# Optimization experiments

Measured on AMD Instinct MI355X. Metric: run time of the kernel, lower is better.

## Reference

```python
import jax, jax.numpy as jnp
import numpy as np

B, N, DIM, H = 2, 1024, 512, 8
DK = DIM // H
HIDDEN = 16
EPS = 1e-6
BETA_NOT = 0.5


def setup_inputs() -> dict:
    key = jax.random.key(0)
    ks = jax.random.split(key, 8)
    s = 0.02
    return {
        "x": jax.random.normal(ks[0], (B, N, DIM), jnp.float32),
        "Wqkv0": jax.random.normal(ks[1], (DIM, 3 * DIM), jnp.float32) * s,
        "Wqkv1": jax.random.normal(ks[2], (DIM, 3 * DIM), jnp.float32) * s,
        "Wproj": jax.random.normal(ks[3], (DIM, DIM), jnp.float32) * s,
        "conv1_w": jax.random.normal(ks[4], (HIDDEN, 6), jnp.float32) * s,  # 1x1 conv, 6 in-ch
        "conv1_b": jnp.zeros((HIDDEN,), jnp.float32),
        "conv2_w": jax.random.normal(ks[5], (4, HIDDEN), jnp.float32) * s,  # 1x1 conv -> 4 gates
        "conv2_b": jnp.full((4,), -5.0, jnp.float32),  # gate_init='neutral': all biases -5
        "chain_value_logit": jnp.asarray(-2.0, jnp.float32),
    }


def reference(x, Wqkv0, Wqkv1, Wproj, conv1_w, conv1_b, conv2_w, conv2_b, chain_value_logit):
    scale = 1.0 / np.sqrt(DK).astype(np.float32)

    def qkv(W):
        t = (x @ W).reshape(B, N, 3, H, DK).transpose(2, 0, 3, 1, 4)  # [3,B,H,N,dk]
        return t[0], t[1], t[2]

    q0, k0, v0 = qkv(Wqkv0)
    q1, k1, v1 = qkv(Wqkv1)

    S0 = jnp.einsum('bhnd,bhmd->bhnm', q0, k0) * scale
    S1 = jnp.einsum('bhnd,bhmd->bhnm', q1, k1) * scale
    A0 = jax.nn.softmax(S0, axis=-1)
    A1 = jax.nn.softmax(S1, axis=-1)
    C_fwd = A0 @ A1
    C_bwd = A1 @ A0

    BtH = B * H
    S0i = S0.reshape(BtH, N, N)
    S1i = S1.reshape(BtH, N, N)
    Cri = jnp.log(C_fwd + EPS).reshape(BtH, N, N)
    Cli = jnp.log(C_bwd + EPS).reshape(BtH, N, N)
    # channels: [S1..SM, S1^T..SM^T, log C_fwd, log C_bwd]
    feat = jnp.stack([S0i, S1i, S0i.transpose(0, 2, 1), S1i.transpose(0, 2, 1), Cri, Cli], axis=1)

    # dense edge-gate head: 1x1 conv -> GELU(tanh) -> 1x1 conv -> sigmoid
    h1 = jax.nn.gelu(jnp.einsum('bcnm,oc->bonm', feat, conv1_w) + conv1_b[None, :, None, None],
                     approximate=True)
    gates = jax.nn.sigmoid(jnp.einsum('bcnm,oc->bonm', h1, conv2_w) + conv2_b[None, :, None, None])
    g_and, g_or, g_not, g_chain = gates[:, 0], gates[:, 1], gates[:, 2], gates[:, 3]

    lse_all = jnp.logaddexp(S0i, S1i)  # logsumexp over the 2 views
    # n_views=2: S_sum-S0 = S1, S_mean_others = S1
    Smix = S0i + g_and * S1i + g_or * (lse_all - S0i) - g_not * (BETA_NOT * S1i) + g_chain * Cri

    A = jax.nn.softmax(Smix.reshape(B, H, N, N), axis=-1)
    y_base = A @ v0
    y_chain = A0 @ (A1 @ v1)  # value-aware chain transport
    y = y_base + jax.nn.sigmoid(chain_value_logit) * y_chain
    y = y.transpose(0, 2, 1, 3).reshape(B, N, DIM)
    return y @ Wproj
```

## Files before the change

### kernel.cpp

```cpp
#include <hip/hip_runtime.h>
#include <math.h>
#include <stdio.h>


typedef unsigned short u16;
typedef __attribute__((ext_vector_type(8))) short short8;
typedef __attribute__((ext_vector_type(4))) short short4v;
typedef __attribute__((ext_vector_type(4))) float f32x4;
typedef __attribute__((ext_vector_type(2))) float f32x2;
typedef __attribute__((ext_vector_type(16))) float f32x16;

#define DEVI static __device__ __forceinline__

DEVI float bf2f(u16 u){ union{unsigned v; float f;} x; x.v = ((unsigned)u)<<16u; return x.f; }
DEVI u16 f2bf(float f){ union{float f; unsigned v;} x; x.f=f; unsigned r = x.v + 0x7FFFu + ((x.v>>16)&1u); return (u16)(r>>16); }

DEVI f32x2 bc(float s){ f32x2 r; r[0]=s; r[1]=s; return r; }
DEVI f32x2 pkfma(f32x2 a, f32x2 b, f32x2 c){ return __builtin_elementwise_fma(a,b,c); }
DEVI f32x2 pkmin(f32x2 a, f32x2 b){ return __builtin_elementwise_min(a,b); }
DEVI f32x2 pkmax(f32x2 a, f32x2 b){ return __builtin_elementwise_max(a,b); }

DEVI void gload_lds16(const u16* gptr, u16* lptr){
  __builtin_amdgcn_global_load_lds(
      (const __attribute__((address_space(1))) void*)gptr,
      (__attribute__((address_space(3))) void*)lptr,
      16, 0, 0);
}

enum { EPI_F32=0, EPI_BF16=1, EPI_LOGBF16=2, EPI_BF16T=3, EPI_QKV=4, EPI_Y=5 };

template<int BM,int BN,int WR,int WC,int EPI,int MODE>
__global__ __launch_bounds__(256) void gemm_bt(
    const u16* __restrict__ A, const u16* __restrict__ B,
    const u16* __restrict__ A2, const u16* __restrict__ B2,
    void* __restrict__ p0, void* __restrict__ p1, void* __restrict__ p2,
    void* __restrict__ p0b, void* __restrict__ p1b, void* __restrict__ p2b,
    const float* __restrict__ logit,
    int K, int lda, int ldb,
    long long sA, long long sB, long long sC, int ldc, int zsplit)
{
  constexpr int WM = BM/WR, WN = BN/WC;
  constexpr int MB = WM/32, NB = WN/32;
  constexpr int BK = 64;
  __shared__ u16 As[BM][BK];
  __shared__ u16 Bs[BN][BK];
  const int z = blockIdx.z;
  const bool sec = (MODE==1) && (z >= zsplit);
  const int ze = sec ? z - zsplit : z;
  const u16* Ap = (sec ? A2 : A) + (long long)ze*sA;
  const u16* Bp = (sec ? B2 : B) + (long long)ze*sB;
  void* o0 = sec ? p0b : p0;
  void* o1 = sec ? p1b : p1;
  void* o2 = sec ? p2b : p2;
  const int r0 = blockIdx.y*BM, c0 = blockIdx.x*BN;
  const int tid = threadIdx.x;
  const int wave = tid>>6, lane = tid&63;
  const int wr = (wave/WC)*WM, wc = (wave%WC)*WN;
  const int lrow = lane&31;
  const int kby  = (lane>>5)*16;
  const int l8 = lane>>3, l7 = lane&7;
  const int scol = ((l7 ^ l8) * 8);

  f32x16 acc[MB][NB] = {};

  auto kloop = [&](const u16* AP, const u16* BP){
    for (int k0=0; k0<K; k0+=BK){
      __syncthreads();
      #pragma unroll
      for (int i=0;i<BM/32;i++){
        int ins = wave + 4*i;
        int row = ins*8 + l8;
        gload_lds16(&AP[(long long)(r0+row)*lda + k0 + scol], &As[ins*8][0]);
      }
      #pragma unroll
      for (int i=0;i<BN/32;i++){
        int ins = wave + 4*i;
        int row = ins*8 + l8;
        gload_lds16(&BP[(long long)(c0+row)*ldb + k0 + scol], &Bs[ins*8][0]);
      }
      __syncthreads();
      #pragma unroll
      for (int kk=0; kk<4; ++kk){
        short8 af[MB], bfr[NB];
        #pragma unroll
        for (int m=0;m<MB;m++){
          int R = wr + m*32 + lrow;
          int eo = ((kk*32 + kby) ^ ((R&7)<<4)) >> 1;
          af[m] = *(const short8*)&As[R][eo];
        }
        #pragma unroll
        for (int n=0;n<NB;n++){
          int R = wc + n*32 + lrow;
          int eo = ((kk*32 + kby) ^ ((R&7)<<4)) >> 1;
          bfr[n] = *(const short8*)&Bs[R][eo];
        }
        #pragma unroll
        for (int m=0;m<MB;m++)
          #pragma unroll
          for (int n=0;n<NB;n++)
            acc[m][n] = __builtin_amdgcn_mfma_f32_32x32x16_bf16(af[m], bfr[n], acc[m][n], 0,0,0);
      }
    }
  };

  kloop(Ap, Bp);
  if constexpr (MODE==2){
    kloop(A2 + (long long)z*sA, B2 + (long long)z*sB);
  }

  float tscale = 1.f;
  if constexpr (EPI==EPI_BF16T){ if (logit) tscale = 1.f/(1.f+expf(-logit[0])); }

  #pragma unroll
  for (int m=0;m<MB;m++)
   #pragma unroll
   for (int n=0;n<NB;n++)
    #pragma unroll
    for (int reg=0;reg<16;reg++){
      int r = r0 + wr + m*32 + (reg&3) + 8*(reg>>2) + 4*(lane>>5);
      int c = c0 + wc + n*32 + lrow;
      float v = acc[m][n][reg];
      if constexpr (EPI==EPI_F32){
        ((float*)o0)[(long long)z*sC + (long long)r*ldc + c] = v;
      } else if constexpr (EPI==EPI_BF16){
        ((u16*)o0)[(long long)ze*sC + (long long)r*ldc + c] = f2bf(v);
      } else if constexpr (EPI==EPI_LOGBF16){
        ((u16*)o0)[(long long)z*sC + (long long)r*ldc + c] = f2bf(__logf(v + 1e-6f));
      } else if constexpr (EPI==EPI_BF16T){
        ((u16*)o0)[(long long)z*sC + (long long)c*ldc + r] = f2bf(v*tscale);
      } else if constexpr (EPI==EPI_QKV){
        int b = r>>10, n_ = r&1023;
        int which = c>>9, h = (c>>6)&7, d = c&63;
        long long bh = (long long)b*8 + h;
        if (which==0)      ((u16*)o0)[(bh*1024 + n_)*64 + d] = f2bf(v*0.125f);
        else if (which==1) ((u16*)o1)[(bh*1024 + n_)*64 + d] = f2bf(v);
        else               ((u16*)o2)[(bh*64 + d)*1024 + n_] = f2bf(v);
      } else if constexpr (EPI==EPI_Y){
        int b = z>>3, h = z&7;
        ((u16*)o0)[((long long)(b*1024 + r))*512 + h*64 + c] = f2bf(v);
      }
    }
}

__global__ __launch_bounds__(256) void softmaxT(
    const u16* __restrict__ Sa, u16* __restrict__ Aa, u16* __restrict__ ATa,
    const u16* __restrict__ Sb, u16* __restrict__ Ab2, u16* __restrict__ ATb)
{
  __shared__ u16 tile[32][1032];
  const int zz = blockIdx.y;
  const long long nn = 1048576;
  const u16* S; u16 *A; u16 *AT;
  if (zz < 16){ S = Sa + (long long)zz*nn;      A = Aa  + (long long)zz*nn;      AT = ATa + (long long)zz*nn; }
  else        { S = Sb + (long long)(zz-16)*nn; A = Ab2 + (long long)(zz-16)*nn; AT = ATb + (long long)(zz-16)*nn; }
  const int rb = blockIdx.x*32;
  const int tid = threadIdx.x;

  #pragma unroll
  for (int i=0;i<16;i++){
    int f = tid + i*256;
    int r = f>>7, c = (f&127)*8;
    *(short8*)&tile[r][c] = *(const short8*)&S[(long long)(rb+r)*1024 + c];
  }
  __syncthreads();

  const int row = ((tid>>6)<<3) + ((tid&63)>>3);
  const int seg = tid&7;
  float m = -3.4e38f;
  #pragma unroll
  for (int j=0;j<16;j++){
    short8 x = *(const short8*)&tile[row][seg*128 + j*8];
    #pragma unroll
    for (int q=0;q<8;q++) m = fmaxf(m, bf2f((u16)x[q]));
  }
  m = fmaxf(m, __shfl_xor(m,1,64));
  m = fmaxf(m, __shfl_xor(m,2,64));
  m = fmaxf(m, __shfl_xor(m,4,64));
  float s = 0.f;
  #pragma unroll
  for (int j=0;j<16;j++){
    short8 x = *(const short8*)&tile[row][seg*128 + j*8];
    #pragma unroll
    for (int q=0;q<8;q++) s += __expf(bf2f((u16)x[q]) - m);
  }
  s += __shfl_xor(s,1,64);
  s += __shfl_xor(s,2,64);
  s += __shfl_xor(s,4,64);
  float inv = 1.f/s;
  #pragma unroll
  for (int j=0;j<16;j++){
    short8 x = *(const short8*)&tile[row][seg*128 + j*8];
    short8 o;
    #pragma unroll
    for (int q=0;q<8;q++) o[q] = (short)f2bf(__expf(bf2f((u16)x[q]) - m)*inv);
    *(short8*)&tile[row][seg*128 + j*8] = o;
  }
  __syncthreads();
  #pragma unroll
  for (int i=0;i<16;i++){
    int f = tid + i*256;
    int r = f>>7, c = (f&127)*8;
    *(short8*)&A[(long long)(rb+r)*1024 + c] = *(const short8*)&tile[r][c];
  }
  #pragma unroll
  for (int i=0;i<4;i++){
    int c = tid*4 + i;
    short8 o0, o1, o2, o3;
    #pragma unroll
    for (int q=0;q<8;q++){
      o0[q] = (short)tile[q][c];
      o1[q] = (short)tile[8+q][c];
      o2[q] = (short)tile[16+q][c];
      o3[q] = (short)tile[24+q][c];
    }
    u16* dst = &AT[(long long)c*1024 + rb];
    *(short8*)&dst[0]  = o0;
    *(short8*)&dst[8]  = o1;
    *(short8*)&dst[16] = o2;
    *(short8*)&dst[24] = o3;
  }
}

__global__ __launch_bounds__(256) void softmax_rows2(
    const u16* __restrict__ s0, u16* __restrict__ d0,
    const u16* __restrict__ s1, u16* __restrict__ d1, int half)
{
  const int b = blockIdx.x;
  const u16* s; u16* a;
  if (b < half){ s = s0 + (long long)b*1024;        a = d0 + (long long)b*1024; }
  else         { s = s1 + (long long)(b-half)*1024; a = d1 + (long long)(b-half)*1024; }
  const int tid = threadIdx.x;
  short4v x = *(const short4v*)&s[tid*4];
  float v[4];
  #pragma unroll
  for (int i=0;i<4;i++) v[i] = bf2f((u16)x[i]);
  __shared__ float red[4];
  float m = fmaxf(fmaxf(v[0],v[1]),fmaxf(v[2],v[3]));
  #pragma unroll
  for (int off=32; off>0; off>>=1) m = fmaxf(m, __shfl_xor(m, off, 64));
  if ((tid&63)==0) red[tid>>6] = m;
  __syncthreads();
  m = fmaxf(fmaxf(red[0],red[1]),fmaxf(red[2],red[3]));
  float e[4], sum=0.f;
  #pragma unroll
  for (int i=0;i<4;i++){ e[i] = __expf(v[i]-m); sum += e[i]; }
  #pragma unroll
  for (int off=32; off>0; off>>=1) sum += __shfl_xor(sum, off, 64);
  __syncthreads();
  if ((tid&63)==0) red[tid>>6] = sum;
  __syncthreads();
  float inv = 1.f/(red[0]+red[1]+red[2]+red[3]);
  short4v o;
  #pragma unroll
  for (int i=0;i<4;i++) o[i] = (short)f2bf(e[i]*inv);
  *(short4v*)&a[tid*4] = o;
}

__global__ __launch_bounds__(256) void cast_f32_bf16(const float* __restrict__ in, u16* __restrict__ out, int n4)
{
  int i = blockIdx.x*256 + threadIdx.x;
  if (i < n4){
    f32x4 x = ((const f32x4*)in)[i];
    short4v o;
    #pragma unroll
    for (int j=0;j<4;j++) o[j] = (short)f2bf(x[j]);
    ((short4v*)out)[i] = o;
  }
}

__global__ __launch_bounds__(256) void castT_f32_bf16_2(
    const float* __restrict__ in0, u16* __restrict__ out0,
    const float* __restrict__ in1, u16* __restrict__ out1, int rows, int cols)
{
  __shared__ float tile[32][33];
  const float* in = blockIdx.z ? in1 : in0;
  u16* out        = blockIdx.z ? out1 : out0;
  const int cb = blockIdx.x*32, rb = blockIdx.y*32;
  const int tx = threadIdx.x&31, ty = threadIdx.x>>5;
  #pragma unroll
  for (int rr=0;rr<4;rr++){
    int i = ty + rr*8;
    tile[i][tx] = in[(long long)(rb+i)*cols + cb+tx];
  }
  __syncthreads();
  #pragma unroll
  for (int rr=0;rr<4;rr++){
    int i = ty + rr*8;
    out[(long long)(cb+i)*rows + rb+tx] = f2bf(tile[tx][i]);
  }
}

__global__ __launch_bounds__(256) void castT_f32_bf16(const float* __restrict__ in, u16* __restrict__ out, int rows, int cols)
{
  __shared__ float tile[32][33];
  const int cb = blockIdx.x*32, rb = blockIdx.y*32;
  const int tx = threadIdx.x&31, ty = threadIdx.x>>5;
  #pragma unroll
  for (int rr=0;rr<4;rr++){
    int i = ty + rr*8;
    tile[i][tx] = in[(long long)(rb+i)*cols + cb+tx];
  }
  __syncthreads();
  #pragma unroll
  for (int rr=0;rr<4;rr++){
    int i = ty + rr*8;
    out[(long long)(cb+i)*rows + rb+tx] = f2bf(tile[tx][i]);
  }
}

__global__ __launch_bounds__(256) void gating_kernel(
    const u16* __restrict__ S0, const u16* __restrict__ S1,
    const u16* __restrict__ CR, const u16* __restrict__ CL,
    const float* __restrict__ w1, const float* __restrict__ b1,
    const float* __restrict__ w2, const float* __restrict__ b2,
    u16* __restrict__ Smix)
{
  __shared__ float t0[32][33], t1[32][33], t0t[32][33], t1t[32][33];
  const int tid = threadIdx.x;
  const long long base = (long long)blockIdx.z*1024*1024;
  const int rb = blockIdx.y*32, cb = blockIdx.x*32;
  const int tx = tid&31, ty = tid>>5;
  #pragma unroll
  for (int rr=0;rr<4;rr++){
    int i = ty + rr*8;
    t0 [i][tx] = bf2f(S0[base + (long long)(rb+i)*1024 + cb+tx]);
    t1 [i][tx] = bf2f(S1[base + (long long)(rb+i)*1024 + cb+tx]);
    t0t[i][tx] = bf2f(S0[base + (long long)(cb+i)*1024 + rb+tx]);
    t1t[i][tx] = bf2f(S1[base + (long long)(cb+i)*1024 + rb+tx]);
  }
  __syncthreads();
  #pragma unroll 1
  for (int rr=0;rr<2;rr++){
    const int i0 = ty + rr*16, i1 = i0 + 8;
    f32x2 s0, s1v, s0t, s1t, cr, cl;
    s0[0]  = t0 [i0][tx]; s0[1]  = t0 [i1][tx];
    s1v[0] = t1 [i0][tx]; s1v[1] = t1 [i1][tx];
    s0t[0] = t0t[tx][i0]; s0t[1] = t0t[tx][i1];
    s1t[0] = t1t[tx][i0]; s1t[1] = t1t[tx][i1];
    long long off0 = base + (long long)(rb+i0)*1024 + cb+tx;
    long long off1 = base + (long long)(rb+i1)*1024 + cb+tx;
    cr[0] = bf2f(CR[off0]); cr[1] = bf2f(CR[off1]);
    cl[0] = bf2f(CL[off0]); cl[1] = bf2f(CL[off1]);
    f32x2 a0 = bc(b2[0]), a1 = bc(b2[1]), a2 = bc(b2[2]), a3 = bc(b2[3]);
    #pragma unroll 4
    for (int o=0;o<16;o++){
      f32x2 xx = pkfma(bc(w1[o*6+0]), s0,  bc(b1[o]));
      xx = pkfma(bc(w1[o*6+1]), s1v, xx);
      xx = pkfma(bc(w1[o*6+2]), s0t, xx);
      xx = pkfma(bc(w1[o*6+3]), s1t, xx);
      xx = pkfma(bc(w1[o*6+4]), cr,  xx);
      xx = pkfma(bc(w1[o*6+5]), cl,  xx);
      f32x2 xx2 = xx*xx;
      f32x2 u   = pkfma(bc(0.044715f), xx2, bc(1.f));
      f32x2 zz  = (xx*u) * bc(1.5957691f);
      zz = pkmin(pkmax(zz, bc(-3.f)), bc(3.f));
      f32x2 w   = pkfma(bc(-0.011008f), zz*zz, bc(0.25f));
      f32x2 p   = pkfma(zz, w, bc(0.5f));
      f32x2 hh  = xx*p;
      a0 = pkfma(bc(w2[o]),    hh, a0);
      a1 = pkfma(bc(w2[16+o]), hh, a1);
      a2 = pkfma(bc(w2[32+o]), hh, a2);
      a3 = pkfma(bc(w2[48+o]), hh, a3);
    }
    f32x2 g0, g1, g2, g3;
    { float E;
      E=__expf(a0[0]); g0[0]=E*(1.f-E);  E=__expf(a0[1]); g0[1]=E*(1.f-E);
      E=__expf(a1[0]); g1[0]=E*(1.f-E);  E=__expf(a1[1]); g1[1]=E*(1.f-E);
      E=__expf(a2[0]); g2[0]=E*(1.f-E);  E=__expf(a2[1]); g2[1]=E*(1.f-E);
      E=__expf(a3[0]); g3[0]=E*(1.f-E);  E=__expf(a3[1]); g3[1]=E*(1.f-E);
    }
    f32x2 mx = pkmax(s0, s1v);
    f32x2 dd = s0 - s1v;
    f32x2 ad = pkmax(dd, bc(0.f)-dd);
    f32x2 ee, lg;
    ee[0] = __expf(-ad[0]); ee[1] = __expf(-ad[1]);
    lg[0] = __logf(1.f+ee[0]); lg[1] = __logf(1.f+ee[1]);
    f32x2 lse = mx + lg;
    f32x2 smix = s0 + g0*s1v + g1*(lse - s0) - g2*(bc(0.5f)*s1v) + g3*cr;
    Smix[off0] = f2bf(smix[0]);
    Smix[off1] = f2bf(smix[1]);
  }
}

extern "C" void kernel_launch(void* const* d_in, const int* in_sizes, int n_in,
                              void* d_out, int out_size, void* d_ws, size_t ws_size,
                              hipStream_t stream)
{
  const float* x     = (const float*)d_in[0];
  const float* Wqkv0 = (const float*)d_in[1];
  const float* Wqkv1 = (const float*)d_in[2];
  const float* Wproj = (const float*)d_in[3];
  const float* c1w   = (const float*)d_in[4];
  const float* c1b   = (const float*)d_in[5];
  const float* c2w   = (const float*)d_in[6];
  const float* c2b   = (const float*)d_in[7];
  const float* logit = (const float*)d_in[8];

  char* ws = (char*)d_ws;
  size_t off = 0;
  auto alloc = [&](size_t bytes)->char*{ char* p = ws + off; off = (off + bytes + 255) & ~(size_t)255; return p; };

  const long long NN16 = 16LL*1024*1024;
  u16* xb  = (u16*)alloc(2048LL*512*2);
  u16* w0T = (u16*)alloc(1536LL*512*2);
  u16* w1T = (u16*)alloc(1536LL*512*2);
  u16* wpT = (u16*)alloc(512LL*512*2);
  u16* q0  = (u16*)alloc(16LL*1024*64*2);
  u16* k0  = (u16*)alloc(16LL*1024*64*2);
  u16* v0T = (u16*)alloc(16LL*1024*64*2);
  u16* q1  = (u16*)alloc(16LL*1024*64*2);
  u16* k1  = (u16*)alloc(16LL*1024*64*2);
  u16* v1T = (u16*)alloc(16LL*1024*64*2);
  u16* S0b = (u16*)alloc(NN16*2);
  u16* S1b = (u16*)alloc(NN16*2);
  u16* A0  = (u16*)alloc(NN16*2);
  u16* A1  = (u16*)alloc(NN16*2);
  u16* A0T = (u16*)alloc(NN16*2);
  u16* A1T = (u16*)alloc(NN16*2);
  u16* CL  = (u16*)alloc(NN16*2);
  u16* tT  = (u16*)alloc(16LL*64*1024*2);
  u16* Yb  = (u16*)alloc(2048LL*512*2);

  u16* CR   = A0T;
  u16* Smix = A1T;
  u16* Ab   = S0b;

  if (off > ws_size){
    fprintf(stderr, "kernel_launch: ws too small: need %zu have %zu\n", off, ws_size);
    return;
  }

  dim3 blk(256);

  cast_f32_bf16<<<dim3(262144/256), blk, 0, stream>>>(x, xb, 262144);
  castT_f32_bf16_2<<<dim3(48,16,2), blk, 0, stream>>>(Wqkv0, w0T, Wqkv1, w1T, 512, 1536);
  castT_f32_bf16<<<dim3(16,16), blk, 0, stream>>>(Wproj, wpT, 512, 512);

  gemm_bt<128,128,2,2,EPI_QKV,1><<<dim3(12,16,2), blk, 0, stream>>>(
      xb, w0T, xb, w1T, q0, k0, v0T, q1, k1, v1T, nullptr,
      512, 512, 512, 0, 0, 0, 0, 1);

  gemm_bt<128,128,2,2,EPI_BF16,1><<<dim3(8,8,32), blk, 0, stream>>>(
      q0, k0, q1, k1, S0b, nullptr, nullptr, S1b, nullptr, nullptr, nullptr,
      64, 64, 64, 65536, 65536, 1048576, 1024, 16);

  softmaxT<<<dim3(32,32), blk, 0, stream>>>(S0b, A0, A0T, S1b, A1, A1T);

  gemm_bt<128,128,2,2,EPI_LOGBF16,0><<<dim3(8,8,16), blk, 0, stream>>>(
      A1, A0T, nullptr, nullptr, CL, nullptr, nullptr, nullptr, nullptr, nullptr, nullptr,
      1024, 1024, 1024, 1048576, 1048576, 1048576, 1024, 0);
  gemm_bt<128,128,2,2,EPI_LOGBF16,0><<<dim3(8,8,16), blk, 0, stream>>>(
      A0, A1T, nullptr, nullptr, CR, nullptr, nullptr, nullptr, nullptr, nullptr, nullptr,
      1024, 1024, 1024, 1048576, 1048576, 1048576, 1024, 0);

  gating_kernel<<<dim3(32,32,16), blk, 0, stream>>>(S0b, S1b, CR, CL, c1w, c1b, c2w, c2b, Smix);

  softmax_rows2<<<dim3(16384), blk, 0, stream>>>(Smix, Ab, Smix, Ab, 16384);

  gemm_bt<64,64,2,2,EPI_BF16T,0><<<dim3(1,16,16), blk, 0, stream>>>(
      A1, v1T, nullptr, nullptr, tT, nullptr, nullptr, nullptr, nullptr, nullptr, logit,
      1024, 1024, 1024, 1048576, 65536, 65536, 1024, 0);

  gemm_bt<64,64,2,2,EPI_Y,2><<<dim3(1,16,16), blk, 0, stream>>>(
      Ab, v0T, A0, tT, Yb, nullptr, nullptr, nullptr, nullptr, nullptr, nullptr,
      1024, 1024, 1024, 1048576, 65536, 0, 0, 0);

  gemm_bt<64,64,2,2,EPI_F32,0><<<dim3(8,32,1), blk, 0, stream>>>(
      Yb, wpT, nullptr, nullptr, d_out, nullptr, nullptr, nullptr, nullptr, nullptr, nullptr,
      512, 512, 512, 0, 0, 0, 512, 0);

  (void)in_sizes; (void)n_in; (void)out_size;
}
```

Before: 382.9 us.

## Reuse C_fwd for chain values, fold log into gating, wave-per-row softmax

Computes y_chain as C_fwd @ v1 using the already-materialised A0@A1 product (stored raw in bf16, not as its log), and drops the separate A1@v1 GEMM and its temporary. The chain sigmoid scale moves into the QKV epilogue on v1. The log(C+eps) is now evaluated inside the gating kernel, and the row softmax uses one wave per row with no LDS reductions or barriers. Storing C in bf16 before the log and reassociating the product can change numerics.

```diff
diff --git a/kernel.cpp b/kernel.cpp
--- a/kernel.cpp
+++ b/kernel.cpp
@@ -27,7 +27,7 @@
       16, 0, 0);
 }
 
-enum { EPI_F32=0, EPI_BF16=1, EPI_LOGBF16=2, EPI_BF16T=3, EPI_QKV=4, EPI_Y=5 };
+enum { EPI_F32=0, EPI_BF16=1, EPI_QKV=4, EPI_Y=5 };
 
 template<int BM,int BN,int WR,int WC,int EPI,int MODE>
 __global__ __launch_bounds__(256) void gemm_bt(
@@ -108,8 +108,8 @@
     kloop(A2 + (long long)z*sA, B2 + (long long)z*sB);
   }
 
-  float tscale = 1.f;
-  if constexpr (EPI==EPI_BF16T){ if (logit) tscale = 1.f/(1.f+expf(-logit[0])); }
+  float vscale = 1.f;
+  if constexpr (EPI==EPI_QKV){ if (logit && sec) vscale = 1.f/(1.f+expf(-logit[0])); }
 
   #pragma unroll
   for (int m=0;m<MB;m++)
@@ -124,17 +124,13 @@
         ((float*)o0)[(long long)z*sC + (long long)r*ldc + c] = v;
       } else if constexpr (EPI==EPI_BF16){
         ((u16*)o0)[(long long)ze*sC + (long long)r*ldc + c] = f2bf(v);
-      } else if constexpr (EPI==EPI_LOGBF16){
-        ((u16*)o0)[(long long)z*sC + (long long)r*ldc + c] = f2bf(__logf(v + 1e-6f));
-      } else if constexpr (EPI==EPI_BF16T){
-        ((u16*)o0)[(long long)z*sC + (long long)c*ldc + r] = f2bf(v*tscale);
       } else if constexpr (EPI==EPI_QKV){
         int b = r>>10, n_ = r&1023;
         int which = c>>9, h = (c>>6)&7, d = c&63;
         long long bh = (long long)b*8 + h;
         if (which==0)      ((u16*)o0)[(bh*1024 + n_)*64 + d] = f2bf(v*0.125f);
         else if (which==1) ((u16*)o1)[(bh*1024 + n_)*64 + d] = f2bf(v);
-        else               ((u16*)o2)[(bh*64 + d)*1024 + n_] = f2bf(v);
+        else               ((u16*)o2)[(bh*64 + d)*1024 + n_] = f2bf(v*vscale);
       } else if constexpr (EPI==EPI_Y){
         int b = z>>3, h = z&7;
         ((u16*)o0)[((long long)(b*1024 + r))*512 + h*64 + c] = f2bf(v);
@@ -220,39 +216,34 @@
   }
 }
 
-__global__ __launch_bounds__(256) void softmax_rows2(
-    const u16* __restrict__ s0, u16* __restrict__ d0,
-    const u16* __restrict__ s1, u16* __restrict__ d1, int half)
-{
-  const int b = blockIdx.x;
-  const u16* s; u16* a;
-  if (b < half){ s = s0 + (long long)b*1024;        a = d0 + (long long)b*1024; }
-  else         { s = s1 + (long long)(b-half)*1024; a = d1 + (long long)(b-half)*1024; }
-  const int tid = threadIdx.x;
-  short4v x = *(const short4v*)&s[tid*4];
-  float v[4];
-  #pragma unroll
-  for (int i=0;i<4;i++) v[i] = bf2f((u16)x[i]);
-  __shared__ float red[4];
-  float m = fmaxf(fmaxf(v[0],v[1]),fmaxf(v[2],v[3]));
+__global__ __launch_bounds__(256) void softmax_wave(
+    const u16* __restrict__ S, u16* __restrict__ A)
+{
+  const int wave = threadIdx.x>>6, lane = threadIdx.x&63;
+  const long long row = (long long)blockIdx.x*4 + wave;
+  const u16* s = S + row*1024;
+  u16* a = A + row*1024;
+  short8 x0 = *(const short8*)&s[lane*16];
+  short8 x1 = *(const short8*)&s[lane*16+8];
+  float v[16];
+  #pragma unroll
+  for (int q=0;q<8;q++){ v[q]=bf2f((u16)x0[q]); v[8+q]=bf2f((u16)x1[q]); }
+  float m = v[0];
+  #pragma unroll
+  for (int q=1;q<16;q++) m = fmaxf(m, v[q]);
   #pragma unroll
   for (int off=32; off>0; off>>=1) m = fmaxf(m, __shfl_xor(m, off, 64));
-  if ((tid&63)==0) red[tid>>6] = m;
-  __syncthreads();
-  m = fmaxf(fmaxf(red[0],red[1]),fmaxf(red[2],red[3]));
-  float e[4], sum=0.f;
-  #pragma unroll
-  for (int i=0;i<4;i++){ e[i] = __expf(v[i]-m); sum += e[i]; }
+  float sum = 0.f;
+  #pragma unroll
+  for (int q=0;q<16;q++){ v[q] = __expf(v[q]-m); sum += v[q]; }
   #pragma unroll
   for (int off=32; off>0; off>>=1) sum += __shfl_xor(sum, off, 64);
-  __syncthreads();
-  if ((tid&63)==0) red[tid>>6] = sum;
-  __syncthreads();
-  float inv = 1.f/(red[0]+red[1]+red[2]+red[3]);
-  short4v o;
-  #pragma unroll
-  for (int i=0;i<4;i++) o[i] = (short)f2bf(e[i]*inv);
-  *(short4v*)&a[tid*4] = o;
+  float inv = 1.f/sum;
+  short8 o0, o1;
+  #pragma unroll
+  for (int q=0;q<8;q++){ o0[q]=(short)f2bf(v[q]*inv); o1[q]=(short)f2bf(v[8+q]*inv); }
+  *(short8*)&a[lane*16]   = o0;
+  *(short8*)&a[lane*16+8] = o1;
 }
 
 __global__ __launch_bounds__(256) void cast_f32_bf16(const float* __restrict__ in, u16* __restrict__ out, int n4)
@@ -338,8 +329,8 @@
     s1t[0] = t1t[tx][i0]; s1t[1] = t1t[tx][i1];
     long long off0 = base + (long long)(rb+i0)*1024 + cb+tx;
     long long off1 = base + (long long)(rb+i1)*1024 + cb+tx;
-    cr[0] = bf2f(CR[off0]); cr[1] = bf2f(CR[off1]);
-    cl[0] = bf2f(CL[off0]); cl[1] = bf2f(CL[off1]);
+    cr[0] = __logf(bf2f(CR[off0]) + 1e-6f); cr[1] = __logf(bf2f(CR[off1]) + 1e-6f);
+    cl[0] = __logf(bf2f(CL[off0]) + 1e-6f); cl[1] = __logf(bf2f(CL[off1]) + 1e-6f);
     f32x2 a0 = bc(b2[0]), a1 = bc(b2[1]), a2 = bc(b2[2]), a3 = bc(b2[3]);
     #pragma unroll 4
     for (int o=0;o<16;o++){
@@ -417,7 +408,6 @@
   u16* A0T = (u16*)alloc(NN16*2);
   u16* A1T = (u16*)alloc(NN16*2);
   u16* CL  = (u16*)alloc(NN16*2);
-  u16* tT  = (u16*)alloc(16LL*64*1024*2);
   u16* Yb  = (u16*)alloc(2048LL*512*2);
 
   u16* CR   = A0T;
@@ -436,7 +426,7 @@
   castT_f32_bf16<<<dim3(16,16), blk, 0, stream>>>(Wproj, wpT, 512, 512);
 
   gemm_bt<128,128,2,2,EPI_QKV,1><<<dim3(12,16,2), blk, 0, stream>>>(
-      xb, w0T, xb, w1T, q0, k0, v0T, q1, k1, v1T, nullptr,
+      xb, w0T, xb, w1T, q0, k0, v0T, q1, k1, v1T, logit,
       512, 512, 512, 0, 0, 0, 0, 1);
 
   gemm_bt<128,128,2,2,EPI_BF16,1><<<dim3(8,8,32), blk, 0, stream>>>(
@@ -445,23 +435,19 @@
 
   softmaxT<<<dim3(32,32), blk, 0, stream>>>(S0b, A0, A0T, S1b, A1, A1T);
 
-  gemm_bt<128,128,2,2,EPI_LOGBF16,0><<<dim3(8,8,16), blk, 0, stream>>>(
+  gemm_bt<128,128,2,2,EPI_BF16,0><<<dim3(8,8,16), blk, 0, stream>>>(
       A1, A0T, nullptr, nullptr, CL, nullptr, nullptr, nullptr, nullptr, nullptr, nullptr,
       1024, 1024, 1024, 1048576, 1048576, 1048576, 1024, 0);
-  gemm_bt<128,128,2,2,EPI_LOGBF16,0><<<dim3(8,8,16), blk, 0, stream>>>(
+  gemm_bt<128,128,2,2,EPI_BF16,0><<<dim3(8,8,16), blk, 0, stream>>>(
       A0, A1T, nullptr, nullptr, CR, nullptr, nullptr, nullptr, nullptr, nullptr, nullptr,
       1024, 1024, 1024, 1048576, 1048576, 1048576, 1024, 0);
 
   gating_kernel<<<dim3(32,32,16), blk, 0, stream>>>(S0b, S1b, CR, CL, c1w, c1b, c2w, c2b, Smix);
 
-  softmax_rows2<<<dim3(16384), blk, 0, stream>>>(Smix, Ab, Smix, Ab, 16384);
-
-  gemm_bt<64,64,2,2,EPI_BF16T,0><<<dim3(1,16,16), blk, 0, stream>>>(
-      A1, v1T, nullptr, nullptr, tT, nullptr, nullptr, nullptr, nullptr, nullptr, logit,
-      1024, 1024, 1024, 1048576, 65536, 65536, 1024, 0);
+  softmax_wave<<<dim3(4096), blk, 0, stream>>>(Smix, Ab);
 
   gemm_bt<64,64,2,2,EPI_Y,2><<<dim3(1,16,16), blk, 0, stream>>>(
-      Ab, v0T, A0, tT, Yb, nullptr, nullptr, nullptr, nullptr, nullptr, nullptr,
+      Ab, v0T, CR, v1T, Yb, nullptr, nullptr, nullptr, nullptr, nullptr, nullptr,
       1024, 1024, 1024, 1048576, 65536, 0, 0, 0);
 
   gemm_bt<64,64,2,2,EPI_F32,0><<<dim3(8,32,1), blk, 0, stream>>>(
```

After: 371.4 us. -3.0%, faster.
